# Kernel optimization log

Hardware: AMD Instinct MI355X
Metric: run time of the kernel (lower is better)

Reference implementation:

```python
import math
import jax, jax.numpy as jnp
import numpy as np

FS = 96000.0
N_BIQUADS = 16
HPF_FREQ_RANGE = (20.0, 500.0)
LPF_FREQ_RANGE = (5000.0, 20000.0)
SHELF_FREQ_RANGE = (50.0, 16000.0)
PEAK_FREQ_RANGE = (100.0, 15000.0)
Q_RANGE = (0.5, 16.0)
GAIN_RANGE = (-24.0, 24.0)
BROADBAND_RANGE = (-60.0, 0.0)


def _denorm_log(norm, lo, hi):
    return jnp.exp(math.log(lo) + norm * (math.log(hi) - math.log(lo)))


def _coef_highpass(fc, Q):
    w0 = 2.0 * math.pi * fc / FS
    alpha = jnp.sin(w0) / (2.0 * Q)
    c = jnp.cos(w0)
    b0 = (1 + c) / 2; b1 = -(1 + c); b2 = (1 + c) / 2
    a0 = 1 + alpha; a1 = -2 * c; a2 = 1 - alpha
    return b0 / a0, b1 / a0, b2 / a0, a1 / a0, a2 / a0


def _coef_lowpass(fc, Q):
    w0 = 2.0 * math.pi * fc / FS
    alpha = jnp.sin(w0) / (2.0 * Q)
    c = jnp.cos(w0)
    b0 = (1 - c) / 2; b1 = 1 - c; b2 = (1 - c) / 2
    a0 = 1 + alpha; a1 = -2 * c; a2 = 1 - alpha
    return b0 / a0, b1 / a0, b2 / a0, a1 / a0, a2 / a0


def _coef_lowshelf(fc, gain_db, Q):
    A = 10.0 ** (gain_db / 40.0)
    w0 = 2.0 * math.pi * fc / FS
    alpha = jnp.sin(w0) / (2.0 * Q)
    c = jnp.cos(w0)
    sA = jnp.sqrt(A)
    b0 = A * (A + 1 - (A - 1) * c + 2 * sA * alpha)
    b1 = 2 * A * (A - 1 - (A + 1) * c)
    b2 = A * (A + 1 - (A - 1) * c - 2 * sA * alpha)
    a0 = A + 1 + (A - 1) * c + 2 * sA * alpha
    a1 = -2 * (A - 1 + (A + 1) * c)
    a2 = A + 1 + (A - 1) * c - 2 * sA * alpha
    return b0 / a0, b1 / a0, b2 / a0, a1 / a0, a2 / a0


def _coef_highshelf(fc, gain_db, Q):
    A = 10.0 ** (gain_db / 40.0)
    w0 = 2.0 * math.pi * fc / FS
    alpha = jnp.sin(w0) / (2.0 * Q)
    c = jnp.cos(w0)
    sA = jnp.sqrt(A)
    b0 = A * (A + 1 + (A - 1) * c + 2 * sA * alpha)
    b1 = -2 * A * (A - 1 + (A + 1) * c)
    b2 = A * (A + 1 + (A - 1) * c - 2 * sA * alpha)
    a0 = A + 1 - (A - 1) * c + 2 * sA * alpha
    a1 = 2 * (A - 1 - (A + 1) * c)
    a2 = A + 1 - (A - 1) * c - 2 * sA * alpha
    return b0 / a0, b1 / a0, b2 / a0, a1 / a0, a2 / a0


def _coef_peak(fc, gain_db, Q):
    A = 10.0 ** (gain_db / 40.0)
    w0 = 2.0 * math.pi * fc / FS
    alpha = jnp.sin(w0) / (2.0 * Q)
    c = jnp.cos(w0)
    b0 = 1 + alpha * A; b1 = -2 * c; b2 = 1 - alpha * A
    a0 = 1 + alpha / A; a1 = -2 * c; a2 = 1 - alpha / A
    return b0 / a0, b1 / a0, b2 / a0, a1 / a0, a2 / a0


def _biquad(x, coefs):
    # x: (B, T); coefs: 5 arrays of shape (B,)
    b0, b1, b2, a1, a2 = coefs

    def step(carry, xt):  # xt: (B,)
        s1, s2 = carry
        y = b0 * xt + s1
        return (b1 * xt - a1 * y + s2, b2 * xt - a2 * y), y

    z = jnp.zeros(x.shape[0], x.dtype)
    _, ys = jax.lax.scan(step, (z, z), x.T)  # ys: (T, B)
    return ys.T


def _chain(audio, params):
    B = audio.shape[0]
    bp = params[:, :N_BIQUADS * 3].reshape(B, N_BIQUADS, 3)
    bb_lo, bb_hi = BROADBAND_RANGE
    in_db = bb_lo + params[:, -2] * (bb_hi - bb_lo)
    out_db = bb_lo + params[:, -1] * (bb_hi - bb_lo)
    x = audio * (10.0 ** (in_db / 20.0))[:, None]

    for i in range(N_BIQUADS):
        fn, gn, qn = bp[:, i, 0], bp[:, i, 1], bp[:, i, 2]
        Q = _denorm_log(qn, *Q_RANGE)
        gain = GAIN_RANGE[0] + gn * (GAIN_RANGE[1] - GAIN_RANGE[0])
        if i == 0:  # HPF
            coefs = _coef_highpass(_denorm_log(fn, *HPF_FREQ_RANGE), Q)
        elif i == 15:  # LPF
            coefs = _coef_lowpass(_denorm_log(fn, *LPF_FREQ_RANGE), Q)
        elif i == 1:  # low shelf
            coefs = _coef_lowshelf(_denorm_log(fn, *SHELF_FREQ_RANGE), gain, Q)
        elif i == 14:  # high shelf
            coefs = _coef_highshelf(_denorm_log(fn, *SHELF_FREQ_RANGE), gain, Q)
        else:  # peaking EQ
            coefs = _coef_peak(_denorm_log(fn, *PEAK_FREQ_RANGE), gain, Q)
        x = _biquad(x, coefs)

    return x * (10.0 ** (out_db / 20.0))[:, None]


def setup_inputs() -> dict:
    key = jax.random.key(0)
    k1, k2 = jax.random.split(key)
    audio = jax.random.normal(k1, (16, 262144), dtype=jnp.float32)
    params = jax.random.uniform(k2, (16, 50), dtype=jnp.float32)
    return {"audio": audio, "params": params}


def reference(audio, params):
    return _chain(audio, params)
```

## Files before the change

### kernel.cpp

```cpp
#include <hip/hip_runtime.h>
#include <math.h>

#define BATCH   16
#define T_LEN   262144
#define NB      16
#define L       64
#define GRP     64
#define SUB     16
#define CHAINS  4
#define NSUB    256
#define NSUP    16
#define NG      64
#define NCHUNK  4096

#define DPI 3.14159265358979323846264338327950288

#define OFF_COEF  0
#define OFF_A64   1536
#define OFF_A1K   17920
#define OFF_A16K  34304
#define OFF_QEND  50688
#define OFF_SARR  181760
#define OFF_P     312832

__device__ inline void stage_coefs(int i, double fn, double gn, double qn,
                                   double& B0, double& B1, double& B2,
                                   double& A1, double& A2) {
    const double FS = 96000.0;
    double Q    = exp(log(0.5) + qn * (log(16.0) - log(0.5)));
    double gain = -24.0 + gn * 48.0;
    double lo, hi;
    if (i == 0)            { lo = 20.0;   hi = 500.0;   }
    else if (i == 15)      { lo = 5000.0; hi = 20000.0; }
    else if (i == 1 || i == 14) { lo = 50.0; hi = 16000.0; }
    else                   { lo = 100.0;  hi = 15000.0; }
    double fc    = exp(log(lo) + fn * (log(hi) - log(lo)));
    double w0    = 2.0 * DPI * fc / FS;
    double alpha = sin(w0) / (2.0 * Q);
    double c     = cos(w0);
    double b0, b1, b2, a0, a1, a2;
    if (i == 0) {
        b0 = (1.0 + c) * 0.5; b1 = -(1.0 + c); b2 = (1.0 + c) * 0.5;
        a0 = 1.0 + alpha; a1 = -2.0 * c; a2 = 1.0 - alpha;
    } else if (i == 15) {
        b0 = (1.0 - c) * 0.5; b1 = 1.0 - c; b2 = (1.0 - c) * 0.5;
        a0 = 1.0 + alpha; a1 = -2.0 * c; a2 = 1.0 - alpha;
    } else if (i == 1) {
        double A = pow(10.0, gain / 40.0), sA = sqrt(A);
        b0 = A * ((A + 1.0) - (A - 1.0) * c + 2.0 * sA * alpha);
        b1 = 2.0 * A * ((A - 1.0) - (A + 1.0) * c);
        b2 = A * ((A + 1.0) - (A - 1.0) * c - 2.0 * sA * alpha);
        a0 = (A + 1.0) + (A - 1.0) * c + 2.0 * sA * alpha;
        a1 = -2.0 * ((A - 1.0) + (A + 1.0) * c);
        a2 = (A + 1.0) + (A - 1.0) * c - 2.0 * sA * alpha;
    } else if (i == 14) {
        double A = pow(10.0, gain / 40.0), sA = sqrt(A);
        b0 = A * ((A + 1.0) + (A - 1.0) * c + 2.0 * sA * alpha);
        b1 = -2.0 * A * ((A - 1.0) + (A + 1.0) * c);
        b2 = A * ((A + 1.0) + (A - 1.0) * c - 2.0 * sA * alpha);
        a0 = (A + 1.0) - (A - 1.0) * c + 2.0 * sA * alpha;
        a1 = 2.0 * ((A - 1.0) - (A + 1.0) * c);
        a2 = (A + 1.0) - (A - 1.0) * c - 2.0 * sA * alpha;
    } else {
        double A = pow(10.0, gain / 40.0);
        b0 = 1.0 + alpha * A; b1 = -2.0 * c; b2 = 1.0 - alpha * A;
        a0 = 1.0 + alpha / A; a1 = -2.0 * c; a2 = 1.0 - alpha / A;
    }
    B0 = b0 / a0; B1 = b1 / a0; B2 = b2 / a0; A1 = a1 / a0; A2 = a2 / a0;
}

__global__ __launch_bounds__(256) void k0_setup(const float* __restrict__ params,
                                                float* __restrict__ coefs,
                                                float* __restrict__ A64,
                                                float* __restrict__ A1K,
                                                float* __restrict__ A16K) {
    int b = blockIdx.x;
    int t = threadIdx.x;
    __shared__ double cf[NB][5];
    __shared__ double M1[32 * 32];
    __shared__ double M2[32 * 32];

    if (t < NB) {
        double B0, B1, B2, A1, A2;
        stage_coefs(t, (double)params[b * 50 + t * 3 + 0],
                       (double)params[b * 50 + t * 3 + 1],
                       (double)params[b * 50 + t * 3 + 2], B0, B1, B2, A1, A2);
        float f0 = (float)B0, f1 = (float)B1, f2 = (float)B2, f3 = (float)A1, f4 = (float)A2;
        cf[t][0] = (double)f0; cf[t][1] = (double)f1; cf[t][2] = (double)f2;
        cf[t][3] = (double)f3; cf[t][4] = (double)f4;
        float* cp = coefs + b * 96 + t * 5;
        cp[0] = f0; cp[1] = f1; cp[2] = f2; cp[3] = f3; cp[4] = f4;
    }
    if (t == NB) {
        double indb = -60.0 + (double)params[b * 50 + 48] * 60.0;
        coefs[b * 96 + 80] = (float)pow(10.0, indb / 20.0);
    }
    if (t == NB + 1) {
        double outdb = -60.0 + (double)params[b * 50 + 49] * 60.0;
        coefs[b * 96 + 81] = (float)pow(10.0, outdb / 20.0);
    }
    __syncthreads();

    if (t < 32) {
        double s1[NB], s2[NB];
#pragma unroll
        for (int i = 0; i < NB; i++) {
            s1[i] = (t == 2 * i) ? 1.0 : 0.0;
            s2[i] = (t == 2 * i + 1) ? 1.0 : 0.0;
        }
        double u = 0.0;
#pragma unroll
        for (int i = 0; i < NB; i++) {
            double y  = cf[i][0] * u + s1[i];
            double n1 = cf[i][1] * u - cf[i][3] * y + s2[i];
            double n2 = cf[i][2] * u - cf[i][4] * y;
            s1[i] = n1; s2[i] = n2; u = y;
        }
#pragma unroll
        for (int i = 0; i < NB; i++) {
            M1[(2 * i) * 32 + t]     = s1[i];
            M1[(2 * i + 1) * 32 + t] = s2[i];
        }
    }
    __syncthreads();

    int c  = t & 31;
    int r0 = t >> 5;
    double* src = M1;
    double* dst = M2;
    for (int sq = 0; sq < 14; sq++) {
        double acc[4] = {0.0, 0.0, 0.0, 0.0};
        for (int k = 0; k < 32; k++) {
            double bv = src[k * 32 + c];
#pragma unroll
            for (int e = 0; e < 4; e++)
                acc[e] += src[(e * 8 + r0) * 32 + k] * bv;
        }
#pragma unroll
        for (int e = 0; e < 4; e++) dst[(e * 8 + r0) * 32 + c] = acc[e];
        __syncthreads();
        { double* tmp = src; src = dst; dst = tmp; }
        float* out_m = (sq == 5) ? A64 : (sq == 9) ? A1K : (sq == 13) ? A16K : nullptr;
        if (out_m) {
#pragma unroll
            for (int e = 0; e < 4; e++) {
                int idx = (e * 8 + r0) * 32 + c;
                out_m[b * 1024 + idx] = (float)src[idx];
            }
        }
        __syncthreads();
    }
}

__device__ __forceinline__ float mv_step_rl(const float* ar, float q, float addv) {
    int qi = __float_as_int(q);
    float acc0 = addv, acc1 = 0.f;
#pragma unroll
    for (int t = 0; t < 32; t += 2) {
        float qa = __int_as_float(__builtin_amdgcn_readlane(qi, t));
        float qb = __int_as_float(__builtin_amdgcn_readlane(qi, t + 1));
        acc0 = fmaf(ar[t], qa, acc0);
        acc1 = fmaf(ar[t + 1], qb, acc1);
    }
    return acc0 + acc1;
}

__device__ __forceinline__ void load_row32(const float* base, int row, float* ar) {
    const float4* a4 = (const float4*)(base + row * 32);
#pragma unroll
    for (int j = 0; j < 8; j++) {
        float4 v = a4[j];
        ar[4 * j + 0] = v.x; ar[4 * j + 1] = v.y;
        ar[4 * j + 2] = v.z; ar[4 * j + 3] = v.w;
    }
}

__global__ __launch_bounds__(64, 1) void k1_pass1(const float* __restrict__ audio,
                                                  const float* __restrict__ coefs,
                                                  const float* __restrict__ A64,
                                                  float* __restrict__ P,
                                                  float* __restrict__ Qend) {
    int blk   = blockIdx.x;
    int batch = blk >> 6;
    int grp   = blk & 63;
    int lane  = threadIdx.x;
    int chunk = grp * GRP + lane;
    int row   = lane & 31;

    const float* cf = coefs + batch * 96;
    float c0[NB], c1[NB], c2[NB], c3[NB], c4[NB];
#pragma unroll
    for (int i = 0; i < NB; i++) {
        c0[i] = cf[i * 5 + 0]; c1[i] = cf[i * 5 + 1]; c2[i] = cf[i * 5 + 2];
        c3[i] = cf[i * 5 + 3]; c4[i] = cf[i * 5 + 4];
    }
    float ing = cf[80];

    float s1[NB], s2[NB];
#pragma unroll
    for (int i = 0; i < NB; i++) { s1[i] = 0.f; s2[i] = 0.f; }

    const float4* xp = (const float4*)(audio + (size_t)batch * T_LEN + (size_t)chunk * L);
    float4 cur = xp[0];
    float4 nxt = xp[1];
#pragma unroll 1
    for (int tt = 0; tt < 16; tt++) {
        float4 fut = xp[(tt < 14) ? (tt + 2) : 15];
        float xs[4] = {cur.x, cur.y, cur.z, cur.w};
#pragma unroll
        for (int j = 0; j < 4; j++) {
            float u = ing * xs[j];
#pragma unroll
            for (int i = 0; i < NB; i++) {
                float y  = fmaf(c0[i], u, s1[i]);
                float n1 = fmaf(c1[i], u, s2[i]); n1 = fmaf(-c3[i], y, n1);
                float n2 = c2[i] * u;             n2 = fmaf(-c4[i], y, n2);
                s1[i] = n1; s2[i] = n2; u = y;
            }
        }
        cur = nxt; nxt = fut;
    }

    {
        float* pb = P + ((size_t)(batch * NG + grp)) * 2048;
#pragma unroll
        for (int i = 0; i < NB; i++) {
            pb[(2 * i) * 64 + lane]     = s1[i];
            pb[(2 * i + 1) * 64 + lane] = s2[i];
        }
    }

    __shared__ float plds[GRP][33];
#pragma unroll
    for (int i = 0; i < NB; i++) {
        plds[lane][2 * i]     = s1[i];
        plds[lane][2 * i + 1] = s2[i];
    }
    __syncthreads();

    float ar[32];
    load_row32(A64 + batch * 1024, row, ar);
    float q0 = 0.f, q1 = 0.f, q2 = 0.f, q3 = 0.f;
    float p0 = plds[0 * SUB][row], p1 = plds[1 * SUB][row],
          p2 = plds[2 * SUB][row], p3 = plds[3 * SUB][row];
#pragma unroll 1
    for (int j = 0; j < SUB; j++) {
        float n0 = 0.f, n1 = 0.f, n2 = 0.f, n3 = 0.f;
        if (j < SUB - 1) {
            n0 = plds[0 * SUB + j + 1][row];
            n1 = plds[1 * SUB + j + 1][row];
            n2 = plds[2 * SUB + j + 1][row];
            n3 = plds[3 * SUB + j + 1][row];
        }
        q0 = mv_step_rl(ar, q0, p0);
        q1 = mv_step_rl(ar, q1, p1);
        q2 = mv_step_rl(ar, q2, p2);
        q3 = mv_step_rl(ar, q3, p3);
        p0 = n0; p1 = n1; p2 = n2; p3 = n3;
    }
    if (lane < 32) {
        float* qe = Qend + ((size_t)(batch * NSUB + grp * CHAINS)) * 32 + row;
        qe[0] = q0; qe[32] = q1; qe[64] = q2; qe[96] = q3;
    }
}

__global__ __launch_bounds__(256, 1) void k2_combine(const float* __restrict__ A1K,
                                                     const float* __restrict__ A16K,
                                                     const float* __restrict__ Qend,
                                                     float* __restrict__ Sarr) {
    int batch = blockIdx.x;
    int tid   = threadIdx.x;
    int wave  = tid >> 6;
    int lane  = tid & 63;
    int row   = lane & 31;

    __shared__ float qe[NSUB][32];
    __shared__ float qs[NSUP][32];
    __shared__ float ss[NSUP][32];

    {
        const float4* src4 = (const float4*)(Qend + (size_t)batch * NSUB * 32);
        float4* dst4 = (float4*)&qe[0][0];
        for (int i = tid; i < NSUB * 32 / 4; i += 256) dst4[i] = src4[i];
    }
    float ar1k[32];
    load_row32(A1K + batch * 1024, row, ar1k);
    __syncthreads();

    int s0i = wave * 4;
    {
        float q0 = 0.f, q1 = 0.f, q2 = 0.f, q3 = 0.f;
#pragma unroll 1
        for (int j = 0; j < 16; j++) {
            float p0 = qe[(s0i + 0) * 16 + j][row];
            float p1 = qe[(s0i + 1) * 16 + j][row];
            float p2 = qe[(s0i + 2) * 16 + j][row];
            float p3 = qe[(s0i + 3) * 16 + j][row];
            q0 = mv_step_rl(ar1k, q0, p0);
            q1 = mv_step_rl(ar1k, q1, p1);
            q2 = mv_step_rl(ar1k, q2, p2);
            q3 = mv_step_rl(ar1k, q3, p3);
        }
        if (lane < 32) {
            qs[s0i + 0][row] = q0; qs[s0i + 1][row] = q1;
            qs[s0i + 2][row] = q2; qs[s0i + 3][row] = q3;
        }
    }
    __syncthreads();

    if (wave == 0) {
        float ark[32];
        load_row32(A16K + batch * 1024, row, ark);
        float S = 0.f;
#pragma unroll 1
        for (int s = 0; s < NSUP; s++) {
            if (lane < 32) ss[s][row] = S;
            float addv = qs[s][row];
            S = mv_step_rl(ark, S, addv);
        }
    }
    __syncthreads();

    {
        float q0 = ss[s0i + 0][row];
        float q1 = ss[s0i + 1][row];
        float q2 = ss[s0i + 2][row];
        float q3 = ss[s0i + 3][row];
#pragma unroll 1
        for (int j = 0; j < 16; j++) {
            if (lane < 32) {
                Sarr[((size_t)(batch * NSUB + (s0i + 0) * 16 + j)) * 32 + row] = q0;
                Sarr[((size_t)(batch * NSUB + (s0i + 1) * 16 + j)) * 32 + row] = q1;
                Sarr[((size_t)(batch * NSUB + (s0i + 2) * 16 + j)) * 32 + row] = q2;
                Sarr[((size_t)(batch * NSUB + (s0i + 3) * 16 + j)) * 32 + row] = q3;
            }
            float p0 = qe[(s0i + 0) * 16 + j][row];
            float p1 = qe[(s0i + 1) * 16 + j][row];
            float p2 = qe[(s0i + 2) * 16 + j][row];
            float p3 = qe[(s0i + 3) * 16 + j][row];
            q0 = mv_step_rl(ar1k, q0, p0);
            q1 = mv_step_rl(ar1k, q1, p1);
            q2 = mv_step_rl(ar1k, q2, p2);
            q3 = mv_step_rl(ar1k, q3, p3);
        }
    }
}

__global__ __launch_bounds__(64, 1) void k3_pass2(const float* __restrict__ audio,
                                                  const float* __restrict__ coefs,
                                                  const float* __restrict__ A64,
                                                  const float* __restrict__ P,
                                                  const float* __restrict__ Sarr,
                                                  float* __restrict__ out) {
    int blk   = blockIdx.x;
    int batch = blk >> 6;
    int grp   = blk & 63;
    int lane  = threadIdx.x;
    int chunk = grp * GRP + lane;
    int row   = lane & 31;

    __shared__ float plds[GRP][33];

    {
        const float* pb = P + ((size_t)(batch * NG + grp)) * 2048;
        float pv[32];
#pragma unroll
        for (int s = 0; s < 32; s++) pv[s] = pb[s * 64 + lane];
#pragma unroll
        for (int s = 0; s < 32; s++) plds[lane][s] = pv[s];
    }
    __syncthreads();

    {
        float ar[32];
        load_row32(A64 + batch * 1024, row, ar);
        const float* sp = Sarr + ((size_t)(batch * NSUB + grp * CHAINS)) * 32 + row;
        float q0 = sp[0], q1 = sp[32], q2 = sp[64], q3 = sp[96];
#pragma unroll 1
        for (int j = 0; j < SUB; j++) {
            float p0 = plds[0 * SUB + j][row];
            float p1 = plds[1 * SUB + j][row];
            float p2 = plds[2 * SUB + j][row];
            float p3 = plds[3 * SUB + j][row];
            if (lane < 32) {
                plds[0 * SUB + j][row] = q0;
                plds[1 * SUB + j][row] = q1;
                plds[2 * SUB + j][row] = q2;
                plds[3 * SUB + j][row] = q3;
            }
            q0 = mv_step_rl(ar, q0, p0);
            q1 = mv_step_rl(ar, q1, p1);
            q2 = mv_step_rl(ar, q2, p2);
            q3 = mv_step_rl(ar, q3, p3);
        }
    }
    __syncthreads();

    const float* cf = coefs + batch * 96;
    float c0[NB], c1[NB], c2[NB], c3[NB], c4[NB];
#pragma unroll
    for (int i = 0; i < NB; i++) {
        c0[i] = cf[i * 5 + 0]; c1[i] = cf[i * 5 + 1]; c2[i] = cf[i * 5 + 2];
        c3[i] = cf[i * 5 + 3]; c4[i] = cf[i * 5 + 4];
    }
    float ing  = cf[80];
    float outg = cf[81];

    float s1[NB], s2[NB];
#pragma unroll
    for (int i = 0; i < NB; i++) {
        s1[i] = plds[lane][2 * i];
        s2[i] = plds[lane][2 * i + 1];
    }

    const float4* xp = (const float4*)(audio + (size_t)batch * T_LEN + (size_t)chunk * L);
    float4* yp = (float4*)(out + (size_t)batch * T_LEN + (size_t)chunk * L);
    float4 cur = xp[0];
    float4 nxt = xp[1];
#pragma unroll 1
    for (int tt = 0; tt < 16; tt++) {
        float4 fut = xp[(tt < 14) ? (tt + 2) : 15];
        float xs[4] = {cur.x, cur.y, cur.z, cur.w};
        float ys[4];
#pragma unroll
        for (int j = 0; j < 4; j++) {
            float u = ing * xs[j];
#pragma unroll
            for (int i = 0; i < NB; i++) {
                float y  = fmaf(c0[i], u, s1[i]);
                float n1 = fmaf(c1[i], u, s2[i]); n1 = fmaf(-c3[i], y, n1);
                float n2 = c2[i] * u;             n2 = fmaf(-c4[i], y, n2);
                s1[i] = n1; s2[i] = n2; u = y;
            }
            ys[j] = outg * u;
        }
        float4 yv; yv.x = ys[0]; yv.y = ys[1]; yv.z = ys[2]; yv.w = ys[3];
        yp[tt] = yv;
        cur = nxt; nxt = fut;
    }
}

extern "C" void kernel_launch(void* const* d_in, const int* in_sizes, int n_in,
                              void* d_out, int out_size, void* d_ws, size_t ws_size,
                              hipStream_t stream) {
    const float* audio  = (const float*)d_in[0];
    const float* params = (const float*)d_in[1];
    float* out = (float*)d_out;
    float* ws  = (float*)d_ws;

    float* coefs = ws + OFF_COEF;
    float* A64   = ws + OFF_A64;
    float* A1K   = ws + OFF_A1K;
    float* A16K  = ws + OFF_A16K;
    float* Qend  = ws + OFF_QEND;
    float* Sarr  = ws + OFF_SARR;
    float* P     = ws + OFF_P;

    k0_setup<<<BATCH, 256, 0, stream>>>(params, coefs, A64, A1K, A16K);
    k1_pass1<<<BATCH * NG, 64, 0, stream>>>(audio, coefs, A64, P, Qend);
    k2_combine<<<BATCH, 256, 0, stream>>>(A1K, A16K, Qend, Sarr);
    k3_pass2<<<BATCH * NG, 64, 0, stream>>>(audio, coefs, A64, P, Sarr, out);
}
```

Before: 153.7 us.

## Fuse pass1 and combine kernels via last-block atomic counter

Merges the per-chunk first pass and the per-batch combine step into one kernel. Blocks now hold four waves (four groups each), and the last block to finish for each batch, found through an atomic counter with thread fences, performs the combine. This removes one kernel launch and its inter-kernel gap. In exchange, the combine runs serialized in a single block at the tail, and the 256-thread blocks with larger LDS change occupancy and scheduling.

```diff
diff --git a/kernel.cpp b/kernel.cpp
--- a/kernel.cpp
+++ b/kernel.cpp
@@ -12,6 +12,7 @@
 #define NSUP    16
 #define NG      64
 #define NCHUNK  4096
+#define BPB     16
 
 #define DPI 3.14159265358979323846264338327950288
 
@@ -22,6 +23,7 @@
 #define OFF_QEND  50688
 #define OFF_SARR  181760
 #define OFF_P     312832
+#define OFF_CNT   2409984
 
 __device__ inline void stage_coefs(int i, double fn, double gn, double qn,
                                    double& B0, double& B1, double& B2,
@@ -73,12 +75,15 @@
                                                 float* __restrict__ coefs,
                                                 float* __restrict__ A64,
                                                 float* __restrict__ A1K,
-                                                float* __restrict__ A16K) {
+                                                float* __restrict__ A16K,
+                                                int* __restrict__ cnt) {
     int b = blockIdx.x;
     int t = threadIdx.x;
     __shared__ double cf[NB][5];
     __shared__ double M1[32 * 32];
     __shared__ double M2[32 * 32];
+
+    if (t == 0) cnt[b] = 0;
 
     if (t < NB) {
         double B0, B1, B2, A1, A2;
@@ -175,17 +180,31 @@
     }
 }
 
-__global__ __launch_bounds__(64, 1) void k1_pass1(const float* __restrict__ audio,
-                                                  const float* __restrict__ coefs,
-                                                  const float* __restrict__ A64,
-                                                  float* __restrict__ P,
-                                                  float* __restrict__ Qend) {
+__global__ __launch_bounds__(256, 1) void k1_fused(const float* __restrict__ audio,
+                                                   const float* __restrict__ coefs,
+                                                   const float* __restrict__ A64,
+                                                   const float* __restrict__ A1K,
+                                                   const float* __restrict__ A16K,
+                                                   float* __restrict__ P,
+                                                   float* __restrict__ Qend,
+                                                   float* __restrict__ Sarr,
+                                                   int* __restrict__ cnt) {
+    int tid   = threadIdx.x;
+    int wave  = tid >> 6;
+    int lane  = tid & 63;
+    int row   = lane & 31;
     int blk   = blockIdx.x;
-    int batch = blk >> 6;
-    int grp   = blk & 63;
-    int lane  = threadIdx.x;
+    int batch = blk >> 4;
+    int bgrp  = blk & 15;
+    int grp   = bgrp * 4 + wave;
     int chunk = grp * GRP + lane;
-    int row   = lane & 31;
+
+    __shared__ float lbuf[4 * GRP * 33];
+    __shared__ float qs[NSUP][32];
+    __shared__ float ss[NSUP][32];
+    __shared__ int   lastFlag;
+
+    float (*plds)[33] = (float(*)[33])(lbuf + wave * GRP * 33);
 
     const float* cf = coefs + batch * 96;
     float c0[NB], c1[NB], c2[NB], c3[NB], c4[NB];
@@ -230,54 +249,44 @@
         }
     }
 
-    __shared__ float plds[GRP][33];
 #pragma unroll
     for (int i = 0; i < NB; i++) {
         plds[lane][2 * i]     = s1[i];
         plds[lane][2 * i + 1] = s2[i];
     }
-    __syncthreads();
-
-    float ar[32];
-    load_row32(A64 + batch * 1024, row, ar);
-    float q0 = 0.f, q1 = 0.f, q2 = 0.f, q3 = 0.f;
-    float p0 = plds[0 * SUB][row], p1 = plds[1 * SUB][row],
-          p2 = plds[2 * SUB][row], p3 = plds[3 * SUB][row];
-#pragma unroll 1
-    for (int j = 0; j < SUB; j++) {
-        float n0 = 0.f, n1 = 0.f, n2 = 0.f, n3 = 0.f;
-        if (j < SUB - 1) {
-            n0 = plds[0 * SUB + j + 1][row];
-            n1 = plds[1 * SUB + j + 1][row];
-            n2 = plds[2 * SUB + j + 1][row];
-            n3 = plds[3 * SUB + j + 1][row];
-        }
-        q0 = mv_step_rl(ar, q0, p0);
-        q1 = mv_step_rl(ar, q1, p1);
-        q2 = mv_step_rl(ar, q2, p2);
-        q3 = mv_step_rl(ar, q3, p3);
-        p0 = n0; p1 = n1; p2 = n2; p3 = n3;
-    }
-    if (lane < 32) {
-        float* qe = Qend + ((size_t)(batch * NSUB + grp * CHAINS)) * 32 + row;
-        qe[0] = q0; qe[32] = q1; qe[64] = q2; qe[96] = q3;
-    }
-}
-
-__global__ __launch_bounds__(256, 1) void k2_combine(const float* __restrict__ A1K,
-                                                     const float* __restrict__ A16K,
-                                                     const float* __restrict__ Qend,
-                                                     float* __restrict__ Sarr) {
-    int batch = blockIdx.x;
-    int tid   = threadIdx.x;
-    int wave  = tid >> 6;
-    int lane  = tid & 63;
-    int row   = lane & 31;
-
-    __shared__ float qe[NSUB][32];
-    __shared__ float qs[NSUP][32];
-    __shared__ float ss[NSUP][32];
-
+
+    {
+        float ar[32];
+        load_row32(A64 + batch * 1024, row, ar);
+        float q0 = 0.f, q1 = 0.f, q2 = 0.f, q3 = 0.f;
+#pragma unroll 1
+        for (int j = 0; j < SUB; j++) {
+            float p0 = plds[0 * SUB + j][row];
+            float p1 = plds[1 * SUB + j][row];
+            float p2 = plds[2 * SUB + j][row];
+            float p3 = plds[3 * SUB + j][row];
+            q0 = mv_step_rl(ar, q0, p0);
+            q1 = mv_step_rl(ar, q1, p1);
+            q2 = mv_step_rl(ar, q2, p2);
+            q3 = mv_step_rl(ar, q3, p3);
+        }
+        if (lane < 32) {
+            float* qe = Qend + ((size_t)(batch * NSUB + grp * CHAINS)) * 32 + row;
+            qe[0] = q0; qe[32] = q1; qe[64] = q2; qe[96] = q3;
+        }
+    }
+
+    __syncthreads();
+    if (tid == 0) {
+        __threadfence();
+        int old = atomicAdd(&cnt[batch], 1);
+        lastFlag = (old == BPB - 1) ? 1 : 0;
+    }
+    __syncthreads();
+    if (!lastFlag) return;
+    __threadfence();
+
+    float (*qe)[32] = (float(*)[32])lbuf;
     {
         const float4* src4 = (const float4*)(Qend + (size_t)batch * NSUB * 32);
         float4* dst4 = (float4*)&qe[0][0];
@@ -455,9 +464,10 @@
     float* Qend  = ws + OFF_QEND;
     float* Sarr  = ws + OFF_SARR;
     float* P     = ws + OFF_P;
-
-    k0_setup<<<BATCH, 256, 0, stream>>>(params, coefs, A64, A1K, A16K);
-    k1_pass1<<<BATCH * NG, 64, 0, stream>>>(audio, coefs, A64, P, Qend);
-    k2_combine<<<BATCH, 256, 0, stream>>>(A1K, A16K, Qend, Sarr);
+    int*   cnt   = (int*)(ws + OFF_CNT);
+
+    k0_setup<<<BATCH, 256, 0, stream>>>(params, coefs, A64, A1K, A16K, cnt);
+    k1_fused<<<BATCH * BPB, 256, 0, stream>>>(audio, coefs, A64, A1K, A16K,
+                                              P, Qend, Sarr, cnt);
     k3_pass2<<<BATCH * NG, 64, 0, stream>>>(audio, coefs, A64, P, Sarr, out);
 }
```

New measurement: 161.8 us. 1.05x slower.

## Halve chunk length to 32 samples and double chunk-group parallelism

Applied to the files above, without the earlier changes.

Reduces each thread's sequential chunk from 64 to 32 samples, doubling the number of chunks and blocks per batch (128 groups). The transition-matrix powers are recomputed for the new hierarchy (A^32, A^512, A^8K), and the combine kernel processes twice as many sub-chains per wave. Launch bounds now allow two blocks per CU. This shortens the serial IIR recurrence per thread and raises occupancy, at the cost of more state-propagation matrix-vector work and larger intermediate buffers.

```diff
diff --git a/kernel.cpp b/kernel.cpp
--- a/kernel.cpp
+++ b/kernel.cpp
@@ -4,24 +4,24 @@
 #define BATCH   16
 #define T_LEN   262144
 #define NB      16
-#define L       64
+#define L       32
 #define GRP     64
 #define SUB     16
 #define CHAINS  4
-#define NSUB    256
-#define NSUP    16
-#define NG      64
-#define NCHUNK  4096
+#define NG      128
+#define NCHUNK  8192
+#define NSUB    512
+#define NSUP    32
 
 #define DPI 3.14159265358979323846264338327950288
 
 #define OFF_COEF  0
-#define OFF_A64   1536
-#define OFF_A1K   17920
-#define OFF_A16K  34304
+#define OFF_A32   1536
+#define OFF_A512  17920
+#define OFF_A8K   34304
 #define OFF_QEND  50688
-#define OFF_SARR  181760
-#define OFF_P     312832
+#define OFF_SARR  312832
+#define OFF_P     574976
 
 __device__ inline void stage_coefs(int i, double fn, double gn, double qn,
                                    double& B0, double& B1, double& B2,
@@ -71,9 +71,9 @@
 
 __global__ __launch_bounds__(256) void k0_setup(const float* __restrict__ params,
                                                 float* __restrict__ coefs,
-                                                float* __restrict__ A64,
-                                                float* __restrict__ A1K,
-                                                float* __restrict__ A16K) {
+                                                float* __restrict__ A32,
+                                                float* __restrict__ A512,
+                                                float* __restrict__ A8K) {
     int b = blockIdx.x;
     int t = threadIdx.x;
     __shared__ double cf[NB][5];
@@ -128,7 +128,7 @@
     int r0 = t >> 5;
     double* src = M1;
     double* dst = M2;
-    for (int sq = 0; sq < 14; sq++) {
+    for (int sq = 0; sq < 13; sq++) {
         double acc[4] = {0.0, 0.0, 0.0, 0.0};
         for (int k = 0; k < 32; k++) {
             double bv = src[k * 32 + c];
@@ -140,7 +140,7 @@
         for (int e = 0; e < 4; e++) dst[(e * 8 + r0) * 32 + c] = acc[e];
         __syncthreads();
         { double* tmp = src; src = dst; dst = tmp; }
-        float* out_m = (sq == 5) ? A64 : (sq == 9) ? A1K : (sq == 13) ? A16K : nullptr;
+        float* out_m = (sq == 4) ? A32 : (sq == 8) ? A512 : (sq == 12) ? A8K : nullptr;
         if (out_m) {
 #pragma unroll
             for (int e = 0; e < 4; e++) {
@@ -175,14 +175,14 @@
     }
 }
 
-__global__ __launch_bounds__(64, 1) void k1_pass1(const float* __restrict__ audio,
+__global__ __launch_bounds__(64, 2) void k1_pass1(const float* __restrict__ audio,
                                                   const float* __restrict__ coefs,
-                                                  const float* __restrict__ A64,
+                                                  const float* __restrict__ A32,
                                                   float* __restrict__ P,
                                                   float* __restrict__ Qend) {
     int blk   = blockIdx.x;
-    int batch = blk >> 6;
-    int grp   = blk & 63;
+    int batch = blk >> 7;
+    int grp   = blk & 127;
     int lane  = threadIdx.x;
     int chunk = grp * GRP + lane;
     int row   = lane & 31;
@@ -204,8 +204,8 @@
     float4 cur = xp[0];
     float4 nxt = xp[1];
 #pragma unroll 1
-    for (int tt = 0; tt < 16; tt++) {
-        float4 fut = xp[(tt < 14) ? (tt + 2) : 15];
+    for (int tt = 0; tt < L / 4; tt++) {
+        float4 fut = xp[(tt < L / 4 - 2) ? (tt + 2) : (L / 4 - 1)];
         float xs[4] = {cur.x, cur.y, cur.z, cur.w};
 #pragma unroll
         for (int j = 0; j < 4; j++) {
@@ -239,24 +239,18 @@
     __syncthreads();
 
     float ar[32];
-    load_row32(A64 + batch * 1024, row, ar);
+    load_row32(A32 + batch * 1024, row, ar);
     float q0 = 0.f, q1 = 0.f, q2 = 0.f, q3 = 0.f;
-    float p0 = plds[0 * SUB][row], p1 = plds[1 * SUB][row],
-          p2 = plds[2 * SUB][row], p3 = plds[3 * SUB][row];
 #pragma unroll 1
     for (int j = 0; j < SUB; j++) {
-        float n0 = 0.f, n1 = 0.f, n2 = 0.f, n3 = 0.f;
-        if (j < SUB - 1) {
-            n0 = plds[0 * SUB + j + 1][row];
-            n1 = plds[1 * SUB + j + 1][row];
-            n2 = plds[2 * SUB + j + 1][row];
-            n3 = plds[3 * SUB + j + 1][row];
-        }
+        float p0 = plds[0 * SUB + j][row];
+        float p1 = plds[1 * SUB + j][row];
+        float p2 = plds[2 * SUB + j][row];
+        float p3 = plds[3 * SUB + j][row];
         q0 = mv_step_rl(ar, q0, p0);
         q1 = mv_step_rl(ar, q1, p1);
         q2 = mv_step_rl(ar, q2, p2);
         q3 = mv_step_rl(ar, q3, p3);
-        p0 = n0; p1 = n1; p2 = n2; p3 = n3;
     }
     if (lane < 32) {
         float* qe = Qend + ((size_t)(batch * NSUB + grp * CHAINS)) * 32 + row;
@@ -264,8 +258,8 @@
     }
 }
 
-__global__ __launch_bounds__(256, 1) void k2_combine(const float* __restrict__ A1K,
-                                                     const float* __restrict__ A16K,
+__global__ __launch_bounds__(256, 1) void k2_combine(const float* __restrict__ A512,
+                                                     const float* __restrict__ A8K,
                                                      const float* __restrict__ Qend,
                                                      float* __restrict__ Sarr) {
     int batch = blockIdx.x;
@@ -283,12 +277,13 @@
         float4* dst4 = (float4*)&qe[0][0];
         for (int i = tid; i < NSUB * 32 / 4; i += 256) dst4[i] = src4[i];
     }
-    float ar1k[32];
-    load_row32(A1K + batch * 1024, row, ar1k);
-    __syncthreads();
-
-    int s0i = wave * 4;
-    {
+    float ar512[32];
+    load_row32(A512 + batch * 1024, row, ar512);
+    __syncthreads();
+
+#pragma unroll 1
+    for (int r = 0; r < 2; r++) {
+        int s0i = wave * 8 + r * 4;
         float q0 = 0.f, q1 = 0.f, q2 = 0.f, q3 = 0.f;
 #pragma unroll 1
         for (int j = 0; j < 16; j++) {
@@ -296,10 +291,10 @@
             float p1 = qe[(s0i + 1) * 16 + j][row];
             float p2 = qe[(s0i + 2) * 16 + j][row];
             float p3 = qe[(s0i + 3) * 16 + j][row];
-            q0 = mv_step_rl(ar1k, q0, p0);
-            q1 = mv_step_rl(ar1k, q1, p1);
-            q2 = mv_step_rl(ar1k, q2, p2);
-            q3 = mv_step_rl(ar1k, q3, p3);
+            q0 = mv_step_rl(ar512, q0, p0);
+            q1 = mv_step_rl(ar512, q1, p1);
+            q2 = mv_step_rl(ar512, q2, p2);
+            q3 = mv_step_rl(ar512, q3, p3);
         }
         if (lane < 32) {
             qs[s0i + 0][row] = q0; qs[s0i + 1][row] = q1;
@@ -310,7 +305,7 @@
 
     if (wave == 0) {
         float ark[32];
-        load_row32(A16K + batch * 1024, row, ark);
+        load_row32(A8K + batch * 1024, row, ark);
         float S = 0.f;
 #pragma unroll 1
         for (int s = 0; s < NSUP; s++) {
@@ -321,7 +316,9 @@
     }
     __syncthreads();
 
-    {
+#pragma unroll 1
+    for (int r = 0; r < 2; r++) {
+        int s0i = wave * 8 + r * 4;
         float q0 = ss[s0i + 0][row];
         float q1 = ss[s0i + 1][row];
         float q2 = ss[s0i + 2][row];
@@ -338,23 +335,23 @@
             float p1 = qe[(s0i + 1) * 16 + j][row];
             float p2 = qe[(s0i + 2) * 16 + j][row];
             float p3 = qe[(s0i + 3) * 16 + j][row];
-            q0 = mv_step_rl(ar1k, q0, p0);
-            q1 = mv_step_rl(ar1k, q1, p1);
-            q2 = mv_step_rl(ar1k, q2, p2);
-            q3 = mv_step_rl(ar1k, q3, p3);
-        }
-    }
-}
-
-__global__ __launch_bounds__(64, 1) void k3_pass2(const float* __restrict__ audio,
+            q0 = mv_step_rl(ar512, q0, p0);
+            q1 = mv_step_rl(ar512, q1, p1);
+            q2 = mv_step_rl(ar512, q2, p2);
+            q3 = mv_step_rl(ar512, q3, p3);
+        }
+    }
+}
+
+__global__ __launch_bounds__(64, 2) void k3_pass2(const float* __restrict__ audio,
                                                   const float* __restrict__ coefs,
-                                                  const float* __restrict__ A64,
+                                                  const float* __restrict__ A32,
                                                   const float* __restrict__ P,
                                                   const float* __restrict__ Sarr,
                                                   float* __restrict__ out) {
     int blk   = blockIdx.x;
-    int batch = blk >> 6;
-    int grp   = blk & 63;
+    int batch = blk >> 7;
+    int grp   = blk & 127;
     int lane  = threadIdx.x;
     int chunk = grp * GRP + lane;
     int row   = lane & 31;
@@ -373,7 +370,7 @@
 
     {
         float ar[32];
-        load_row32(A64 + batch * 1024, row, ar);
+        load_row32(A32 + batch * 1024, row, ar);
         const float* sp = Sarr + ((size_t)(batch * NSUB + grp * CHAINS)) * 32 + row;
         float q0 = sp[0], q1 = sp[32], q2 = sp[64], q3 = sp[96];
 #pragma unroll 1
@@ -418,8 +415,8 @@
     float4 cur = xp[0];
     float4 nxt = xp[1];
 #pragma unroll 1
-    for (int tt = 0; tt < 16; tt++) {
-        float4 fut = xp[(tt < 14) ? (tt + 2) : 15];
+    for (int tt = 0; tt < L / 4; tt++) {
+        float4 fut = xp[(tt < L / 4 - 2) ? (tt + 2) : (L / 4 - 1)];
         float xs[4] = {cur.x, cur.y, cur.z, cur.w};
         float ys[4];
 #pragma unroll
@@ -449,15 +446,15 @@
     float* ws  = (float*)d_ws;
 
     float* coefs = ws + OFF_COEF;
-    float* A64   = ws + OFF_A64;
-    float* A1K   = ws + OFF_A1K;
-    float* A16K  = ws + OFF_A16K;
+    float* A32   = ws + OFF_A32;
+    float* A512  = ws + OFF_A512;
+    float* A8K   = ws + OFF_A8K;
     float* Qend  = ws + OFF_QEND;
     float* Sarr  = ws + OFF_SARR;
     float* P     = ws + OFF_P;
 
-    k0_setup<<<BATCH, 256, 0, stream>>>(params, coefs, A64, A1K, A16K);
-    k1_pass1<<<BATCH * NG, 64, 0, stream>>>(audio, coefs, A64, P, Qend);
-    k2_combine<<<BATCH, 256, 0, stream>>>(A1K, A16K, Qend, Sarr);
-    k3_pass2<<<BATCH * NG, 64, 0, stream>>>(audio, coefs, A64, P, Sarr, out);
-}
+    k0_setup<<<BATCH, 256, 0, stream>>>(params, coefs, A32, A512, A8K);
+    k1_pass1<<<BATCH * NG, 64, 0, stream>>>(audio, coefs, A32, P, Qend);
+    k2_combine<<<BATCH, 256, 0, stream>>>(A512, A8K, Qend, Sarr);
+    k3_pass2<<<BATCH * NG, 64, 0, stream>>>(audio, coefs, A32, P, Sarr, out);
+}
```

New measurement: 181.7 us. 1.18x slower.

## Stage audio through LDS with coalesced loads and stores in both passes

Applied to the files above, without the earlier changes.

Both sequential-filter kernels now load their 64 chunks of audio cooperatively with coalesced float4 reads into padded shared memory, and each lane then reads its own chunk from LDS. Pass 2 also writes its outputs back into LDS and stores them to global memory coalesced. Before, each lane streamed its own 256-byte chunk with strided per-lane loads and stores. The matrix-vector readlanes are hoisted into a batch, and the manual prefetch of LDS rows is removed. This costs more LDS and an extra barrier, and the global loads now sit up front instead of overlapping with the filter compute.

```diff
diff --git a/kernel.cpp b/kernel.cpp
--- a/kernel.cpp
+++ b/kernel.cpp
@@ -12,6 +12,7 @@
 #define NSUP    16
 #define NG      64
 #define NCHUNK  4096
+#define XSTRIDE 68
 
 #define DPI 3.14159265358979323846264338327950288
 
@@ -154,13 +155,15 @@
 
 __device__ __forceinline__ float mv_step_rl(const float* ar, float q, float addv) {
     int qi = __float_as_int(q);
+    float qb[32];
+#pragma unroll
+    for (int t = 0; t < 32; t++)
+        qb[t] = __int_as_float(__builtin_amdgcn_readlane(qi, t));
     float acc0 = addv, acc1 = 0.f;
 #pragma unroll
     for (int t = 0; t < 32; t += 2) {
-        float qa = __int_as_float(__builtin_amdgcn_readlane(qi, t));
-        float qb = __int_as_float(__builtin_amdgcn_readlane(qi, t + 1));
-        acc0 = fmaf(ar[t], qa, acc0);
-        acc1 = fmaf(ar[t + 1], qb, acc1);
+        acc0 = fmaf(ar[t], qb[t], acc0);
+        acc1 = fmaf(ar[t + 1], qb[t + 1], acc1);
     }
     return acc0 + acc1;
 }
@@ -172,6 +175,20 @@
         float4 v = a4[j];
         ar[4 * j + 0] = v.x; ar[4 * j + 1] = v.y;
         ar[4 * j + 2] = v.z; ar[4 * j + 3] = v.w;
+    }
+}
+
+__device__ __forceinline__ void stage_audio(const float* __restrict__ gbase,
+                                            float* __restrict__ xlds, int lane) {
+    const float4* g4 = (const float4*)gbase;
+    float4 v[16];
+#pragma unroll
+    for (int it = 0; it < 16; it++) v[it] = g4[it * 64 + lane];
+#pragma unroll
+    for (int it = 0; it < 16; it++) {
+        int idx = it * 64 + lane;
+        int ch = idx >> 4, q = idx & 15;
+        *(float4*)&xlds[ch * XSTRIDE + q * 4] = v[it];
     }
 }
 
@@ -184,8 +201,13 @@
     int batch = blk >> 6;
     int grp   = blk & 63;
     int lane  = threadIdx.x;
-    int chunk = grp * GRP + lane;
     int row   = lane & 31;
+
+    __shared__ float xlds[GRP * XSTRIDE];
+    __shared__ float plds[GRP][33];
+
+    stage_audio(audio + (size_t)batch * T_LEN + (size_t)grp * GRP * L, xlds, lane);
+    __syncthreads();
 
     const float* cf = coefs + batch * 96;
     float c0[NB], c1[NB], c2[NB], c3[NB], c4[NB];
@@ -200,13 +222,11 @@
 #pragma unroll
     for (int i = 0; i < NB; i++) { s1[i] = 0.f; s2[i] = 0.f; }
 
-    const float4* xp = (const float4*)(audio + (size_t)batch * T_LEN + (size_t)chunk * L);
-    float4 cur = xp[0];
-    float4 nxt = xp[1];
+    float* xrow = &xlds[lane * XSTRIDE];
 #pragma unroll 1
     for (int tt = 0; tt < 16; tt++) {
-        float4 fut = xp[(tt < 14) ? (tt + 2) : 15];
-        float xs[4] = {cur.x, cur.y, cur.z, cur.w};
+        float4 xv = *(const float4*)&xrow[tt * 4];
+        float xs[4] = {xv.x, xv.y, xv.z, xv.w};
 #pragma unroll
         for (int j = 0; j < 4; j++) {
             float u = ing * xs[j];
@@ -218,7 +238,6 @@
                 s1[i] = n1; s2[i] = n2; u = y;
             }
         }
-        cur = nxt; nxt = fut;
     }
 
     {
@@ -230,7 +249,6 @@
         }
     }
 
-    __shared__ float plds[GRP][33];
 #pragma unroll
     for (int i = 0; i < NB; i++) {
         plds[lane][2 * i]     = s1[i];
@@ -241,22 +259,16 @@
     float ar[32];
     load_row32(A64 + batch * 1024, row, ar);
     float q0 = 0.f, q1 = 0.f, q2 = 0.f, q3 = 0.f;
-    float p0 = plds[0 * SUB][row], p1 = plds[1 * SUB][row],
-          p2 = plds[2 * SUB][row], p3 = plds[3 * SUB][row];
 #pragma unroll 1
     for (int j = 0; j < SUB; j++) {
-        float n0 = 0.f, n1 = 0.f, n2 = 0.f, n3 = 0.f;
-        if (j < SUB - 1) {
-            n0 = plds[0 * SUB + j + 1][row];
-            n1 = plds[1 * SUB + j + 1][row];
-            n2 = plds[2 * SUB + j + 1][row];
-            n3 = plds[3 * SUB + j + 1][row];
-        }
+        float p0 = plds[0 * SUB + j][row];
+        float p1 = plds[1 * SUB + j][row];
+        float p2 = plds[2 * SUB + j][row];
+        float p3 = plds[3 * SUB + j][row];
         q0 = mv_step_rl(ar, q0, p0);
         q1 = mv_step_rl(ar, q1, p1);
         q2 = mv_step_rl(ar, q2, p2);
         q3 = mv_step_rl(ar, q3, p3);
-        p0 = n0; p1 = n1; p2 = n2; p3 = n3;
     }
     if (lane < 32) {
         float* qe = Qend + ((size_t)(batch * NSUB + grp * CHAINS)) * 32 + row;
@@ -356,10 +368,12 @@
     int batch = blk >> 6;
     int grp   = blk & 63;
     int lane  = threadIdx.x;
-    int chunk = grp * GRP + lane;
     int row   = lane & 31;
 
+    __shared__ float xlds[GRP * XSTRIDE];
     __shared__ float plds[GRP][33];
+
+    stage_audio(audio + (size_t)batch * T_LEN + (size_t)grp * GRP * L, xlds, lane);
 
     {
         const float* pb = P + ((size_t)(batch * NG + grp)) * 2048;
@@ -413,14 +427,11 @@
         s2[i] = plds[lane][2 * i + 1];
     }
 
-    const float4* xp = (const float4*)(audio + (size_t)batch * T_LEN + (size_t)chunk * L);
-    float4* yp = (float4*)(out + (size_t)batch * T_LEN + (size_t)chunk * L);
-    float4 cur = xp[0];
-    float4 nxt = xp[1];
+    float* xrow = &xlds[lane * XSTRIDE];
 #pragma unroll 1
     for (int tt = 0; tt < 16; tt++) {
-        float4 fut = xp[(tt < 14) ? (tt + 2) : 15];
-        float xs[4] = {cur.x, cur.y, cur.z, cur.w};
+        float4 xv = *(const float4*)&xrow[tt * 4];
+        float xs[4] = {xv.x, xv.y, xv.z, xv.w};
         float ys[4];
 #pragma unroll
         for (int j = 0; j < 4; j++) {
@@ -435,8 +446,18 @@
             ys[j] = outg * u;
         }
         float4 yv; yv.x = ys[0]; yv.y = ys[1]; yv.z = ys[2]; yv.w = ys[3];
-        yp[tt] = yv;
-        cur = nxt; nxt = fut;
+        *(float4*)&xrow[tt * 4] = yv;
+    }
+    __syncthreads();
+
+    {
+        float4* g4 = (float4*)(out + (size_t)batch * T_LEN + (size_t)grp * GRP * L);
+#pragma unroll
+        for (int it = 0; it < 16; it++) {
+            int idx = it * 64 + lane;
+            int ch = idx >> 4, q = idx & 15;
+            g4[it * 64 + lane] = *(const float4*)&xlds[ch * XSTRIDE + q * 4];
+        }
     }
 }
 
```

New measurement: 152.1 us (median of 2 runs). No clear change (-1.1%).
